# Kernel optimization log

Measured on AMD Instinct MI355X. Metric: run time of the kernel, lower is better.

## Reference

```python
import jax, jax.numpy as jnp
import numpy as np


def setup_inputs() -> dict:
    key = jax.random.key(0)
    kx, kw, kb = jax.random.split(key, 3)
    x = jax.random.normal(kx, (4, 2048, 4096), dtype=jnp.float32)
    weight = jax.random.normal(kw, (4096, 4096), dtype=jnp.float32) * 0.02
    bias = jax.random.normal(kb, (4096,), dtype=jnp.float32) * 0.02
    return {"x": x, "weight": weight, "bias": bias}


def _binarize_except_outliers(w):
    # Outlier mask from global weight stats (computed from w itself; in torch it
    # is cached after the first call but the values are identical every step).
    mean = jnp.mean(w)
    std = jnp.std(w, ddof=1)  # torch.std default is the unbiased estimator
    lower = mean - 1.96 * std
    upper = mean + 1.96 * std
    outliers = (w < lower) | (w > upper)
    keep = (~outliers).astype(w.dtype)
    # scaling_factor in the torch code: w[~outliers].abs().mean(-1) on the
    # flattened masked-select -> a single SCALAR, detached from the graph.
    scale = jax.lax.stop_gradient(jnp.sum(jnp.abs(w) * keep) / jnp.sum(keep))
    # NOTE: the torch code assigns STE-sign values and then immediately
    # overwrites them with w * scale, so the effective math is:
    w_bin = jnp.where(outliers, w, w * scale)
    return w_bin


def reference(x, weight, bias):
    w_bin = _binarize_except_outliers(weight)  # [out, in]
    # F.linear(x, w, b) = x @ w.T + b
    return jnp.einsum("bsi,oi->bso", x, w_bin) + bias
```

## Files before the change

kernel.cpp:

```cpp
#include <hip/hip_runtime.h>
#include <hip/hip_bf16.h>
#include <math.h>

#define MDIM 8192
#define NDIM 4096
#define KDIM 4096
#define WELEMS 16777216
#define XELEMS 33554432

typedef __attribute__((ext_vector_type(8))) short bf16x8;
typedef __attribute__((ext_vector_type(4))) float f32x4;

__device__ __forceinline__ unsigned short f2bf(float f) {
  unsigned int u = __float_as_uint(f);
  u += 0x7fffu + ((u >> 16) & 1u);
  return (unsigned short)(u >> 16);
}

__device__ __forceinline__ void gload16(const void* g, void* l) {
  __builtin_amdgcn_global_load_lds(
      (const __attribute__((address_space(1))) void*)g,
      (__attribute__((address_space(3))) void*)l, 16, 0, 0);
}


__device__ __forceinline__ float np_tree_reduce(const float* __restrict__ C, float* ls) {
  const int t = threadIdx.x;
  float v[16];
#pragma unroll
  for (int i = 0; i < 16; i++) v[i] = C[t * 16 + i];
#pragma unroll
  for (int n = 16; n > 1; n >>= 1)
    for (int i = 0; i < n / 2; i++) v[i] = v[2 * i] + v[2 * i + 1];
  __syncthreads();
  ls[t] = v[0];
  __syncthreads();
  for (int n = 256; n > 1; n >>= 1) {
    float s = 0.f;
    if (t < n / 2) s = ls[2 * t] + ls[2 * t + 1];
    __syncthreads();
    if (t < n / 2) ls[t] = s;
    __syncthreads();
  }
  float r = ls[0];
  __syncthreads();
  return r;
}

template <int MODE>
__global__ __launch_bounds__(256)
void np_stage1(const float* __restrict__ w, float* __restrict__ C,
               float* __restrict__ C2, const float* __restrict__ scal) {
  __shared__ float ls[32], ls2[32];
  const int t = threadIdx.x;
  const int leaf = t >> 3, j = t & 7;
  const size_t base = (size_t)blockIdx.x * 4096 + leaf * 128 + j;
  float mean = 0.f, lower = 0.f, upper = 0.f;
  if (MODE == 1) mean = scal[0];
  if (MODE == 2) { lower = scal[1]; upper = scal[2]; }
  float r = 0.f, r2 = 0.f;
#pragma unroll
  for (int s = 0; s < 16; s++) {
    float v = w[base + s * 8];
    float tv, tv2 = 0.f;
    if (MODE == 0) tv = v;
    else if (MODE == 1) { float x = v - mean; tv = __fmul_rn(x, x); }
    else {
      bool keep = !(v < lower || v > upper);
      tv = keep ? fabsf(v) : 0.f;
      tv2 = keep ? 1.f : 0.f;
    }
    if (s == 0) { r = tv; r2 = tv2; } else { r += tv; r2 += tv2; }
  }
  r += __shfl_xor(r, 1); r += __shfl_xor(r, 2); r += __shfl_xor(r, 4);
  if (MODE == 2) { r2 += __shfl_xor(r2, 1); r2 += __shfl_xor(r2, 2); r2 += __shfl_xor(r2, 4); }
  if (j == 0) { ls[leaf] = r; if (MODE == 2) ls2[leaf] = r2; }
  __syncthreads();
  if (t == 0) {
    float tmp[32];
    for (int i = 0; i < 32; i++) tmp[i] = ls[i];
    for (int n = 32; n > 1; n >>= 1)
      for (int i = 0; i < n / 2; i++) tmp[i] = tmp[2 * i] + tmp[2 * i + 1];
    C[blockIdx.x] = tmp[0];
    if (MODE == 2) {
      for (int i = 0; i < 32; i++) tmp[i] = ls2[i];
      for (int n = 32; n > 1; n >>= 1)
        for (int i = 0; i < n / 2; i++) tmp[i] = tmp[2 * i] + tmp[2 * i + 1];
      C2[blockIdx.x] = tmp[0];
    }
  }
}

template <int MODE>
__global__ __launch_bounds__(256)
void np_stage2(const float* __restrict__ C, const float* __restrict__ C2,
               float* __restrict__ scal) {
  __shared__ float ls[256], ls2[256];
  const int t = threadIdx.x;
  {
    float v[16];
    for (int i = 0; i < 16; i++) v[i] = C[t * 16 + i];
    for (int n = 16; n > 1; n >>= 1)
      for (int i = 0; i < n / 2; i++) v[i] = v[2 * i] + v[2 * i + 1];
    ls[t] = v[0];
    if (MODE == 2) {
      for (int i = 0; i < 16; i++) v[i] = C2[t * 16 + i];
      for (int n = 16; n > 1; n >>= 1)
        for (int i = 0; i < n / 2; i++) v[i] = v[2 * i] + v[2 * i + 1];
      ls2[t] = v[0];
    }
  }
  __syncthreads();
  if (t == 0) {
    float tmp[256];
    for (int i = 0; i < 256; i++) tmp[i] = ls[i];
    for (int n = 256; n > 1; n >>= 1)
      for (int i = 0; i < n / 2; i++) tmp[i] = tmp[2 * i] + tmp[2 * i + 1];
    float S = tmp[0];
    if (MODE == 0) {
      scal[0] = S / 16777216.0f;
    } else if (MODE == 1) {
      float var = S / 16777215.0f;
      float sd = sqrtf(var);
      float mean = scal[0];
      scal[1] = mean - __fmul_rn(1.96f, sd);
      scal[2] = mean + __fmul_rn(1.96f, sd);
    } else {
      for (int i = 0; i < 256; i++) tmp[i] = ls2[i];
      for (int n = 256; n > 1; n >>= 1)
        for (int i = 0; i < n / 2; i++) tmp[i] = tmp[2 * i] + tmp[2 * i + 1];
      scal[3] = S / tmp[0];
    }
  }
}

__device__ __forceinline__ void pack8(const float* __restrict__ p, unsigned short* dst,
                                      bool dobin, float lower, float upper, float scale) {
  float4 u = *(const float4*)p;
  float4 v = *(const float4*)(p + 4);
  float f[8] = {u.x, u.y, u.z, u.w, v.x, v.y, v.z, v.w};
  unsigned int r[4];
#pragma unroll
  for (int j = 0; j < 4; j++) {
    float a = f[2 * j], b = f[2 * j + 1];
    if (dobin) {
      bool oa = (a < lower) || (a > upper);
      bool ob = (b < lower) || (b > upper);
      a = oa ? a : __fmul_rn(a, scale);
      b = ob ? b : __fmul_rn(b, scale);
    }
    r[j] = (unsigned int)f2bf(a) | ((unsigned int)f2bf(b) << 16);
  }
  *(uint4*)dst = make_uint4(r[0], r[1], r[2], r[3]);
}

__global__ __launch_bounds__(256)
void convert_w(const float* __restrict__ w, unsigned short* __restrict__ wb,
               const float* __restrict__ scal) {
  float lower = scal[1], upper = scal[2], scale = scal[3];
  int tid = blockIdx.x * blockDim.x + threadIdx.x;
  int nth = gridDim.x * blockDim.x;
  int nc = WELEMS / 8;
  for (int i = tid; i < nc; i += nth)
    pack8(w + (size_t)i * 8, wb + (size_t)i * 8, true, lower, upper, scale);
}

__global__ __launch_bounds__(256)
void k2_var_convx(const float* __restrict__ w, const float* __restrict__ x,
                  const float* __restrict__ C1, float* __restrict__ C2,
                  unsigned short* __restrict__ xb) {
  if (blockIdx.x >= 4096) {
    int bid2 = blockIdx.x - 4096;
    for (int i = bid2 * 256 + threadIdx.x; i < XELEMS / 16; i += 2048 * 256)
      pack8(x + (size_t)i * 8, xb + (size_t)i * 8, false, 0.f, 0.f, 0.f);
    return;
  }
  __shared__ float red[256];
  __shared__ float ls[32];
  float mean = np_tree_reduce(C1, red) / 16777216.0f;
  const int t = threadIdx.x;
  const int leaf = t >> 3, j = t & 7;
  const size_t base = (size_t)blockIdx.x * 4096 + leaf * 128 + j;
  float r = 0.f;
#pragma unroll
  for (int s = 0; s < 16; s++) {
    float v = w[base + s * 8];
    float xv = v - mean;
    float tv = __fmul_rn(xv, xv);
    if (s == 0) r = tv; else r += tv;
  }
  r += __shfl_xor(r, 1); r += __shfl_xor(r, 2); r += __shfl_xor(r, 4);
  if (j == 0) ls[leaf] = r;
  __syncthreads();
  if (t == 0) {
    float tmp[32];
    for (int i = 0; i < 32; i++) tmp[i] = ls[i];
    for (int n = 32; n > 1; n >>= 1)
      for (int i = 0; i < n / 2; i++) tmp[i] = tmp[2 * i] + tmp[2 * i + 1];
    C2[blockIdx.x] = tmp[0];
  }
}

__global__ __launch_bounds__(256)
void k3_keep_convx(const float* __restrict__ w, const float* __restrict__ x,
                   const float* __restrict__ C1, const float* __restrict__ C2,
                   float* __restrict__ C3, float* __restrict__ C4,
                   unsigned short* __restrict__ xb) {
  if (blockIdx.x >= 4096) {
    int bid2 = blockIdx.x - 4096;
    for (int i = XELEMS / 16 + bid2 * 256 + threadIdx.x; i < XELEMS / 8; i += 2048 * 256)
      pack8(x + (size_t)i * 8, xb + (size_t)i * 8, false, 0.f, 0.f, 0.f);
    return;
  }
  __shared__ float red[256];
  __shared__ float ls[32], ls2[32];
  float S1 = np_tree_reduce(C1, red);
  float S2 = np_tree_reduce(C2, red);
  float mean = S1 / 16777216.0f;
  float sd = sqrtf(S2 / 16777215.0f);
  float lower = mean - __fmul_rn(1.96f, sd);
  float upper = mean + __fmul_rn(1.96f, sd);
  const int t = threadIdx.x;
  const int leaf = t >> 3, j = t & 7;
  const size_t base = (size_t)blockIdx.x * 4096 + leaf * 128 + j;
  float r = 0.f, r2 = 0.f;
#pragma unroll
  for (int s = 0; s < 16; s++) {
    float v = w[base + s * 8];
    bool keep = !(v < lower || v > upper);
    float tv = keep ? fabsf(v) : 0.f;
    float tv2 = keep ? 1.f : 0.f;
    if (s == 0) { r = tv; r2 = tv2; } else { r += tv; r2 += tv2; }
  }
  r += __shfl_xor(r, 1); r += __shfl_xor(r, 2); r += __shfl_xor(r, 4);
  r2 += __shfl_xor(r2, 1); r2 += __shfl_xor(r2, 2); r2 += __shfl_xor(r2, 4);
  if (j == 0) { ls[leaf] = r; ls2[leaf] = r2; }
  __syncthreads();
  if (t == 0) {
    float tmp[32];
    for (int i = 0; i < 32; i++) tmp[i] = ls[i];
    for (int n = 32; n > 1; n >>= 1)
      for (int i = 0; i < n / 2; i++) tmp[i] = tmp[2 * i] + tmp[2 * i + 1];
    C3[blockIdx.x] = tmp[0];
    for (int i = 0; i < 32; i++) tmp[i] = ls2[i];
    for (int n = 32; n > 1; n >>= 1)
      for (int i = 0; i < n / 2; i++) tmp[i] = tmp[2 * i] + tmp[2 * i + 1];
    C4[blockIdx.x] = tmp[0];
  }
}

__global__ __launch_bounds__(256)
void k4_convw(const float* __restrict__ w, const float* __restrict__ C1,
              const float* __restrict__ C2, const float* __restrict__ C3,
              const float* __restrict__ C4, unsigned short* __restrict__ wb) {
  __shared__ float red[256];
  float S1 = np_tree_reduce(C1, red);
  float S2 = np_tree_reduce(C2, red);
  float S3 = np_tree_reduce(C3, red);
  float S4 = np_tree_reduce(C4, red);
  float mean = S1 / 16777216.0f;
  float sd = sqrtf(S2 / 16777215.0f);
  float lower = mean - __fmul_rn(1.96f, sd);
  float upper = mean + __fmul_rn(1.96f, sd);
  float scale = S3 / S4;
  int tid = blockIdx.x * blockDim.x + threadIdx.x;
  int nth = gridDim.x * blockDim.x;
  int nc = WELEMS / 8;
  for (int i = tid; i < nc; i += nth)
    pack8(w + (size_t)i * 8, wb + (size_t)i * 8, true, lower, upper, scale);
}


#define VM(n) asm volatile("s_waitcnt vmcnt(" #n ")" ::: "memory")
#define PSYNC { asm volatile("" ::: "memory"); __builtin_amdgcn_s_barrier(); asm volatile("" ::: "memory"); }

#define RDA(slot, bufR, h) do { \
  slot[0][0] = *(const bf16x8*)&sA[bufR][wm][((2*(h)  )*16+fr)*64 + koo0]; \
  slot[0][1] = *(const bf16x8*)&sA[bufR][wm][((2*(h)  )*16+fr)*64 + koo1]; \
  slot[1][0] = *(const bf16x8*)&sA[bufR][wm][((2*(h)+1)*16+fr)*64 + koo0]; \
  slot[1][1] = *(const bf16x8*)&sA[bufR][wm][((2*(h)+1)*16+fr)*64 + koo1]; } while (0)

#define RDB2(slot, nf, bufR, bh) do { \
  slot[nf][0] = *(const bf16x8*)&sB[bufR][wnh][(wnq*64+(2*(bh)+(nf))*16+fr)*64 + koo0]; \
  slot[nf][1] = *(const bf16x8*)&sB[bufR][wnh][(wnq*64+(2*(bh)+(nf))*16+fr)*64 + koo1]; } while (0)

#define RDB4(slot, bufR, bh) do { RDB2(slot, 0, bufR, bh); RDB2(slot, 1, bufR, bh); } while (0)

#define MM8(AS, BSL, h, nh) do { \
  __builtin_amdgcn_s_setprio(1); \
  acc[2*(h)  ][2*(nh)  ] = __builtin_amdgcn_mfma_f32_16x16x32_bf16(AS[0][0], BSL[0][0], acc[2*(h)  ][2*(nh)  ], 0, 0, 0); \
  acc[2*(h)  ][2*(nh)+1] = __builtin_amdgcn_mfma_f32_16x16x32_bf16(AS[0][0], BSL[1][0], acc[2*(h)  ][2*(nh)+1], 0, 0, 0); \
  acc[2*(h)+1][2*(nh)  ] = __builtin_amdgcn_mfma_f32_16x16x32_bf16(AS[1][0], BSL[0][0], acc[2*(h)+1][2*(nh)  ], 0, 0, 0); \
  acc[2*(h)+1][2*(nh)+1] = __builtin_amdgcn_mfma_f32_16x16x32_bf16(AS[1][0], BSL[1][0], acc[2*(h)+1][2*(nh)+1], 0, 0, 0); \
  acc[2*(h)  ][2*(nh)  ] = __builtin_amdgcn_mfma_f32_16x16x32_bf16(AS[0][1], BSL[0][1], acc[2*(h)  ][2*(nh)  ], 0, 0, 0); \
  acc[2*(h)  ][2*(nh)+1] = __builtin_amdgcn_mfma_f32_16x16x32_bf16(AS[0][1], BSL[1][1], acc[2*(h)  ][2*(nh)+1], 0, 0, 0); \
  acc[2*(h)+1][2*(nh)  ] = __builtin_amdgcn_mfma_f32_16x16x32_bf16(AS[1][1], BSL[0][1], acc[2*(h)+1][2*(nh)  ], 0, 0, 0); \
  acc[2*(h)+1][2*(nh)+1] = __builtin_amdgcn_mfma_f32_16x16x32_bf16(AS[1][1], BSL[1][1], acc[2*(h)+1][2*(nh)+1], 0, 0, 0); \
  __builtin_amdgcn_s_setprio(0); } while (0)

#define STGA(buf, q, kadd) do { \
  gload16(xbp + aofA[0][q] + (kadd), &sA[buf][0][(q)*4096 + t8]); \
  gload16(xbp + aofA[1][q] + (kadd), &sA[buf][1][(q)*4096 + t8]); } while (0)
#define STGB(buf, h, kadd) do { \
  gload16(wbp + bofB[h][0] + (kadd), &sB[buf][h][t8]); \
  gload16(wbp + bofB[h][1] + (kadd), &sB[buf][h][4096 + t8]); } while (0)

#define TILE(BR, BW, BF, BS_, KADD) do { \
   PSYNC; RDB2(BS_, 0, BR, 1); STGA(BW, 0, KADD); MM8(aA, BF, 0, 0); \
   PSYNC; RDB2(BS_, 1, BR, 1); STGB(BW, 0, KADD); MM8(aB, BF, 1, 0); VM(4); \
   PSYNC; RDA(aC, BR, 2); STGB(BW, 1, KADD); MM8(aB, BS_, 1, 1); \
   PSYNC; RDA(aB, BR, 3); STGA(BW, 1, KADD); MM8(aA, BS_, 0, 1); \
   PSYNC; MM8(aC, BS_, 2, 1); VM(6); \
   PSYNC; RDA(aA, BW, 0); MM8(aB, BS_, 3, 1); VM(2); \
   PSYNC; MM8(aB, BF, 3, 0); RDB4(BS_, BW, 0); \
   PSYNC; MM8(aC, BF, 2, 0); RDA(aB, BW, 1); } while (0)

__global__ __launch_bounds__(512, 2)
void gemm256(const unsigned short* __restrict__ xbp, const unsigned short* __restrict__ wbp,
             const float* __restrict__ bias, float* __restrict__ out) {
  __shared__ unsigned short sA[2][2][8192];
  __shared__ unsigned short sB[2][2][8192];

  const int bid = blockIdx.x;
  const int swz = (bid & 7) * 64 + (bid >> 3);
  const int bm = swz >> 4, bn = swz & 15;

  const int t = threadIdx.x;
  const int lane = t & 63;
  const int wid = t >> 6;
  const int wm = wid >> 2, wn = wid & 3;
  const int wnh = wn >> 1, wnq = wn & 1;
  const int fr = lane & 15;
  const int ko = (lane >> 4) * 8;
  const int xr = (fr & 7) << 3;
  const int koo0 = ko ^ xr;
  const int koo1 = (32 + ko) ^ xr;

  const int t8 = t * 8;
  const int rl = t >> 3;
  const int cs = ((t & 7) * 8) ^ ((rl & 7) << 3);
  unsigned int aofA[2][2], bofB[2][2];
#pragma unroll
  for (int h = 0; h < 2; h++)
#pragma unroll
    for (int q = 0; q < 2; q++) {
      aofA[h][q] = (unsigned int)((bm * 256 + h * 128 + q * 64 + rl) * KDIM + cs);
      bofB[h][q] = (unsigned int)((bn * 256 + h * 128 + q * 64 + rl) * KDIM + cs);
    }

  f32x4 acc[8][4];
#pragma unroll
  for (int i = 0; i < 8; i++)
#pragma unroll
    for (int j = 0; j < 4; j++) acc[i][j] = {0.f, 0.f, 0.f, 0.f};

  bf16x8 aA[2][2], aB[2][2], aC[2][2], bs0[2][2], bs1[2][2];

  STGA(0, 0, 0); STGB(0, 0, 0); STGB(0, 1, 0); STGA(0, 1, 0);
  VM(2); PSYNC;
  RDA(aA, 0, 0); RDA(aB, 0, 1); RDB4(bs0, 0, 0);

  for (int it = 0; it < 31; ++it) {
    TILE(0, 1, bs0, bs1, 64);
    TILE(1, 0, bs1, bs0, 128);
#pragma unroll
    for (int h = 0; h < 2; h++)
#pragma unroll
      for (int q = 0; q < 2; q++) { aofA[h][q] += 128; bofB[h][q] += 128; }
  }
  TILE(0, 1, bs0, bs1, 64);
   PSYNC; RDB2(bs0, 0, 1, 1); MM8(aA, bs1, 0, 0);
   PSYNC; RDB2(bs0, 1, 1, 1); MM8(aB, bs1, 1, 0); VM(0);
   PSYNC; RDA(aC, 1, 2); MM8(aB, bs0, 1, 1);
   PSYNC; RDA(aB, 1, 3); MM8(aA, bs0, 0, 1);
   PSYNC; MM8(aC, bs0, 2, 1);
   PSYNC; MM8(aB, bs0, 3, 1);
   PSYNC; MM8(aB, bs1, 3, 0);
   PSYNC; MM8(aC, bs1, 2, 0);

#pragma unroll
  for (int nn = 0; nn < 4; ++nn) {
    const int col = bn * 256 + wn * 64 + nn * 16 + (lane & 15);
    const float bv = bias[col];
#pragma unroll
    for (int m = 0; m < 8; ++m) {
      const int row0 = bm * 256 + wm * 128 + m * 16 + (lane >> 4) * 4;
#pragma unroll
      for (int q = 0; q < 4; ++q)
        out[(size_t)(row0 + q) * NDIM + col] = acc[m][nn][q] + bv;
    }
  }
}

template <bool A_BF16, bool B_BF16>
__global__ __launch_bounds__(256)
void gemm_bt(const void* __restrict__ Av, const void* __restrict__ Bv,
             const float* __restrict__ bias, float* __restrict__ out,
             const float* __restrict__ scal) {
  __shared__ unsigned short sAt[2][128 * 32];
  __shared__ unsigned short sBt[2][128 * 32];
  float lower = 0.f, upper = 0.f, scale = 0.f;
  if constexpr (!B_BF16) { lower = scal[1]; upper = scal[2]; scale = scal[3]; }
  const unsigned short* Ab = (const unsigned short*)Av;
  const float* Af = (const float*)Av;
  const unsigned short* Bb = (const unsigned short*)Bv;
  const float* Bf = (const float*)Bv;
  int bid = blockIdx.x;
  int swz = (bid & 7) * 256 + (bid >> 3);
  int bm = swz >> 5, bn = swz & 31;
  const int t = threadIdx.x, lane = t & 63, wid = t >> 6;
  const int wm = wid >> 1, wn = wid & 1;
  const int e0 = t * 8, e1 = e0 + 2048;
  const size_t aOff0 = (size_t)(bm * 128 + (e0 >> 5)) * KDIM + (e0 & 31);
  const size_t aOff1 = (size_t)(bm * 128 + (e1 >> 5)) * KDIM + (e1 & 31);
  const size_t bOff0 = (size_t)(bn * 128 + (e0 >> 5)) * KDIM + (e0 & 31);
  const size_t bOff1 = (size_t)(bn * 128 + (e1 >> 5)) * KDIM + (e1 & 31);
  f32x4 acc[4][4];
#pragma unroll
  for (int i = 0; i < 4; i++)
#pragma unroll
    for (int j = 0; j < 4; j++) acc[i][j] = {0.f, 0.f, 0.f, 0.f};
  auto stage = [&](int buf, int k0) {
    if constexpr (A_BF16) {
      gload16(Ab + aOff0 + k0, &sAt[buf][e0]);
      gload16(Ab + aOff1 + k0, &sAt[buf][e1]);
    } else {
      pack8(Af + aOff0 + k0, &sAt[buf][e0], false, 0.f, 0.f, 0.f);
      pack8(Af + aOff1 + k0, &sAt[buf][e1], false, 0.f, 0.f, 0.f);
    }
    if constexpr (B_BF16) {
      gload16(Bb + bOff0 + k0, &sBt[buf][e0]);
      gload16(Bb + bOff1 + k0, &sBt[buf][e1]);
    } else {
      pack8(Bf + bOff0 + k0, &sBt[buf][e0], true, lower, upper, scale);
      pack8(Bf + bOff1 + k0, &sBt[buf][e1], true, lower, upper, scale);
    }
  };
  stage(0, 0);
  const int NT = KDIM / 32;
  const int ko = (lane >> 4) * 8, fr = lane & 15;
  for (int tt = 0; tt < NT; ++tt) {
    int cur = tt & 1;
    __syncthreads();
    if (tt + 1 < NT) stage(cur ^ 1, (tt + 1) * 32);
    bf16x8 a[4], b[4];
#pragma unroll
    for (int i = 0; i < 4; i++) {
      a[i] = *(const bf16x8*)&sAt[cur][(wm * 64 + i * 16 + fr) * 32 + ko];
      b[i] = *(const bf16x8*)&sBt[cur][(wn * 64 + i * 16 + fr) * 32 + ko];
    }
#pragma unroll
    for (int i = 0; i < 4; i++)
#pragma unroll
      for (int j = 0; j < 4; j++)
        acc[i][j] = __builtin_amdgcn_mfma_f32_16x16x32_bf16(a[i], b[j], acc[i][j], 0, 0, 0);
  }
  const int colbase = bn * 128 + wn * 64 + (lane & 15);
  const int rowbase = bm * 128 + wm * 64 + (lane >> 4) * 4;
#pragma unroll
  for (int j = 0; j < 4; j++) {
    int col = colbase + j * 16;
    float bv = bias[col];
#pragma unroll
    for (int i = 0; i < 4; i++) {
      int row0 = rowbase + i * 16;
#pragma unroll
      for (int q = 0; q < 4; q++)
        out[(size_t)(row0 + q) * NDIM + col] = acc[i][j][q] + bv;
    }
  }
}

extern "C" void kernel_launch(void* const* d_in, const int* in_sizes, int n_in,
                              void* d_out, int out_size, void* d_ws, size_t ws_size,
                              hipStream_t stream) {
  const float* x = (const float*)d_in[0];
  const float* w = (const float*)d_in[1];
  const float* bias = (const float*)d_in[2];
  float* out = (float*)d_out;
  char* ws = (char*)d_ws;

  const size_t xb_b = (size_t)XELEMS * 2;
  const size_t wb_b = (size_t)WELEMS * 2;
  const size_t c_b = 4 * 4096 * sizeof(float);
  const bool full = ws_size >= xb_b + wb_b + c_b + 64;
  const bool wonly = !full && ws_size >= wb_b + c_b + 64;

  unsigned short *xb = nullptr, *wb = nullptr;
  float *C1, *scal;
  if (full) {
    xb = (unsigned short*)ws;
    wb = (unsigned short*)(ws + xb_b);
    C1 = (float*)(ws + xb_b + wb_b);
  } else if (wonly) {
    wb = (unsigned short*)ws;
    C1 = (float*)(ws + wb_b);
  } else {
    C1 = (float*)ws;
  }
  float* C2 = C1 + 4096;
  float* C3 = C2 + 4096;
  float* C4 = C3 + 4096;
  scal = C4 + 4096;

  if (full) {
    np_stage1<0><<<dim3(4096), dim3(256), 0, stream>>>(w, C1, nullptr, scal);
    k2_var_convx<<<dim3(6144), dim3(256), 0, stream>>>(w, x, C1, C2, xb);
    k3_keep_convx<<<dim3(6144), dim3(256), 0, stream>>>(w, x, C1, C2, C3, C4, xb);
    k4_convw<<<dim3(2048), dim3(256), 0, stream>>>(w, C1, C2, C3, C4, wb);
    gemm256<<<dim3(512), dim3(512), 0, stream>>>(xb, wb, bias, out);
  } else {
    np_stage1<0><<<dim3(4096), dim3(256), 0, stream>>>(w, C1, nullptr, scal);
    np_stage2<0><<<dim3(1), dim3(256), 0, stream>>>(C1, nullptr, scal);
    np_stage1<1><<<dim3(4096), dim3(256), 0, stream>>>(w, C2, nullptr, scal);
    np_stage2<1><<<dim3(1), dim3(256), 0, stream>>>(C2, nullptr, scal);
    np_stage1<2><<<dim3(4096), dim3(256), 0, stream>>>(w, C3, C4, scal);
    np_stage2<2><<<dim3(1), dim3(256), 0, stream>>>(C3, C4, scal);
    if (wonly) {
      convert_w<<<dim3(2048), dim3(256), 0, stream>>>(w, wb, scal);
      gemm_bt<false, true><<<dim3(2048), dim3(256), 0, stream>>>(x, wb, bias, out, scal);
    } else {
      gemm_bt<false, false><<<dim3(2048), dim3(256), 0, stream>>>(x, w, bias, out, scal);
    }
  }
}
```

Before: 382.7 us.

## Switch GEMM main loop to four-stage K=32 LDS pipeline

Replaces the double-buffered K=64 LDS tiles with a four-buffer ring of K=32 tiles, prefetching three stages ahead with direct global-to-LDS loads. It also changes the LDS swizzle for 32-wide rows and regroups the MFMA schedule into four phases per tile. The aim is to hide global memory latency with deeper prefetch while keeping total LDS size the same. The cost is twice as many barriers per unit of K and a more intricate waitcnt schedule.

```diff
diff --git a/kernel.cpp b/kernel.cpp
--- a/kernel.cpp
+++ b/kernel.cpp
@@ -22,7 +22,6 @@
       (const __attribute__((address_space(1))) void*)g,
       (__attribute__((address_space(3))) void*)l, 16, 0, 0);
 }
-
 
 __device__ __forceinline__ float np_tree_reduce(const float* __restrict__ C, float* ls) {
   const int t = threadIdx.x;
@@ -274,52 +273,46 @@
 #define VM(n) asm volatile("s_waitcnt vmcnt(" #n ")" ::: "memory")
 #define PSYNC { asm volatile("" ::: "memory"); __builtin_amdgcn_s_barrier(); asm volatile("" ::: "memory"); }
 
-#define RDA(slot, bufR, h) do { \
-  slot[0][0] = *(const bf16x8*)&sA[bufR][wm][((2*(h)  )*16+fr)*64 + koo0]; \
-  slot[0][1] = *(const bf16x8*)&sA[bufR][wm][((2*(h)  )*16+fr)*64 + koo1]; \
-  slot[1][0] = *(const bf16x8*)&sA[bufR][wm][((2*(h)+1)*16+fr)*64 + koo0]; \
-  slot[1][1] = *(const bf16x8*)&sA[bufR][wm][((2*(h)+1)*16+fr)*64 + koo1]; } while (0)
-
-#define RDB2(slot, nf, bufR, bh) do { \
-  slot[nf][0] = *(const bf16x8*)&sB[bufR][wnh][(wnq*64+(2*(bh)+(nf))*16+fr)*64 + koo0]; \
-  slot[nf][1] = *(const bf16x8*)&sB[bufR][wnh][(wnq*64+(2*(bh)+(nf))*16+fr)*64 + koo1]; } while (0)
-
-#define RDB4(slot, bufR, bh) do { RDB2(slot, 0, bufR, bh); RDB2(slot, 1, bufR, bh); } while (0)
-
-#define MM8(AS, BSL, h, nh) do { \
+#define RDA4(slot, buf, h) do { \
+  slot[0] = *(const bf16x8*)&sA[buf][wm][((h)*64 +  0 + fr)*32 + koo]; \
+  slot[1] = *(const bf16x8*)&sA[buf][wm][((h)*64 + 16 + fr)*32 + koo]; \
+  slot[2] = *(const bf16x8*)&sA[buf][wm][((h)*64 + 32 + fr)*32 + koo]; \
+  slot[3] = *(const bf16x8*)&sA[buf][wm][((h)*64 + 48 + fr)*32 + koo]; } while (0)
+
+#define RDB2(slot, buf, bh) do { \
+  slot[0] = *(const bf16x8*)&sB[buf][wnh][(wnq*64 + ((bh)*2+0)*16 + fr)*32 + koo]; \
+  slot[1] = *(const bf16x8*)&sB[buf][wnh][(wnq*64 + ((bh)*2+1)*16 + fr)*32 + koo]; } while (0)
+
+#define MMH(AS, BS, mh, n2) do { \
   __builtin_amdgcn_s_setprio(1); \
-  acc[2*(h)  ][2*(nh)  ] = __builtin_amdgcn_mfma_f32_16x16x32_bf16(AS[0][0], BSL[0][0], acc[2*(h)  ][2*(nh)  ], 0, 0, 0); \
-  acc[2*(h)  ][2*(nh)+1] = __builtin_amdgcn_mfma_f32_16x16x32_bf16(AS[0][0], BSL[1][0], acc[2*(h)  ][2*(nh)+1], 0, 0, 0); \
-  acc[2*(h)+1][2*(nh)  ] = __builtin_amdgcn_mfma_f32_16x16x32_bf16(AS[1][0], BSL[0][0], acc[2*(h)+1][2*(nh)  ], 0, 0, 0); \
-  acc[2*(h)+1][2*(nh)+1] = __builtin_amdgcn_mfma_f32_16x16x32_bf16(AS[1][0], BSL[1][0], acc[2*(h)+1][2*(nh)+1], 0, 0, 0); \
-  acc[2*(h)  ][2*(nh)  ] = __builtin_amdgcn_mfma_f32_16x16x32_bf16(AS[0][1], BSL[0][1], acc[2*(h)  ][2*(nh)  ], 0, 0, 0); \
-  acc[2*(h)  ][2*(nh)+1] = __builtin_amdgcn_mfma_f32_16x16x32_bf16(AS[0][1], BSL[1][1], acc[2*(h)  ][2*(nh)+1], 0, 0, 0); \
-  acc[2*(h)+1][2*(nh)  ] = __builtin_amdgcn_mfma_f32_16x16x32_bf16(AS[1][1], BSL[0][1], acc[2*(h)+1][2*(nh)  ], 0, 0, 0); \
-  acc[2*(h)+1][2*(nh)+1] = __builtin_amdgcn_mfma_f32_16x16x32_bf16(AS[1][1], BSL[1][1], acc[2*(h)+1][2*(nh)+1], 0, 0, 0); \
+  acc[(mh)*4+0][(n2)*2+0] = __builtin_amdgcn_mfma_f32_16x16x32_bf16(AS[0], BS[0], acc[(mh)*4+0][(n2)*2+0], 0, 0, 0); \
+  acc[(mh)*4+0][(n2)*2+1] = __builtin_amdgcn_mfma_f32_16x16x32_bf16(AS[0], BS[1], acc[(mh)*4+0][(n2)*2+1], 0, 0, 0); \
+  acc[(mh)*4+1][(n2)*2+0] = __builtin_amdgcn_mfma_f32_16x16x32_bf16(AS[1], BS[0], acc[(mh)*4+1][(n2)*2+0], 0, 0, 0); \
+  acc[(mh)*4+1][(n2)*2+1] = __builtin_amdgcn_mfma_f32_16x16x32_bf16(AS[1], BS[1], acc[(mh)*4+1][(n2)*2+1], 0, 0, 0); \
+  acc[(mh)*4+2][(n2)*2+0] = __builtin_amdgcn_mfma_f32_16x16x32_bf16(AS[2], BS[0], acc[(mh)*4+2][(n2)*2+0], 0, 0, 0); \
+  acc[(mh)*4+2][(n2)*2+1] = __builtin_amdgcn_mfma_f32_16x16x32_bf16(AS[2], BS[1], acc[(mh)*4+2][(n2)*2+1], 0, 0, 0); \
+  acc[(mh)*4+3][(n2)*2+0] = __builtin_amdgcn_mfma_f32_16x16x32_bf16(AS[3], BS[0], acc[(mh)*4+3][(n2)*2+0], 0, 0, 0); \
+  acc[(mh)*4+3][(n2)*2+1] = __builtin_amdgcn_mfma_f32_16x16x32_bf16(AS[3], BS[1], acc[(mh)*4+3][(n2)*2+1], 0, 0, 0); \
   __builtin_amdgcn_s_setprio(0); } while (0)
 
-#define STGA(buf, q, kadd) do { \
-  gload16(xbp + aofA[0][q] + (kadd), &sA[buf][0][(q)*4096 + t8]); \
-  gload16(xbp + aofA[1][q] + (kadd), &sA[buf][1][(q)*4096 + t8]); } while (0)
-#define STGB(buf, h, kadd) do { \
-  gload16(wbp + bofB[h][0] + (kadd), &sB[buf][h][t8]); \
-  gload16(wbp + bofB[h][1] + (kadd), &sB[buf][h][4096 + t8]); } while (0)
-
-#define TILE(BR, BW, BF, BS_, KADD) do { \
-   PSYNC; RDB2(BS_, 0, BR, 1); STGA(BW, 0, KADD); MM8(aA, BF, 0, 0); \
-   PSYNC; RDB2(BS_, 1, BR, 1); STGB(BW, 0, KADD); MM8(aB, BF, 1, 0); VM(4); \
-   PSYNC; RDA(aC, BR, 2); STGB(BW, 1, KADD); MM8(aB, BS_, 1, 1); \
-   PSYNC; RDA(aB, BR, 3); STGA(BW, 1, KADD); MM8(aA, BS_, 0, 1); \
-   PSYNC; MM8(aC, BS_, 2, 1); VM(6); \
-   PSYNC; RDA(aA, BW, 0); MM8(aB, BS_, 3, 1); VM(2); \
-   PSYNC; MM8(aB, BF, 3, 0); RDB4(BS_, BW, 0); \
-   PSYNC; MM8(aC, BF, 2, 0); RDA(aB, BW, 1); } while (0)
+#define STGA32(buf, kadd) do { \
+  gload16(xbp + aof0 + (kadd), &sA[buf][0][t8]); \
+  gload16(xbp + aof1 + (kadd), &sA[buf][1][t8]); } while (0)
+#define STGB32(buf, kadd) do { \
+  gload16(wbp + bof0 + (kadd), &sB[buf][0][t8]); \
+  gload16(wbp + bof1 + (kadd), &sB[buf][1][t8]); } while (0)
+
+#define TILE32(CUR, NXT, STGBUF, BC, BO, DOSTG, KS, DOVM, VMN, DONEXT) do { \
+   PSYNC; RDB2(BO, CUR, 1); if (DOSTG) STGA32(STGBUF, KS); MMH(aX, BC, 0, 0); \
+   PSYNC; RDA4(aY, CUR, 1); MMH(aX, BO, 0, 1); if (DOVM) VM(VMN); \
+   PSYNC; if (DONEXT) RDA4(aX, NXT, 0); if (DOSTG) STGB32(STGBUF, KS); MMH(aY, BO, 1, 1); \
+   PSYNC; if (DONEXT) RDB2(BO, NXT, 0); MMH(aY, BC, 1, 0); } while (0)
 
 __global__ __launch_bounds__(512, 2)
 void gemm256(const unsigned short* __restrict__ xbp, const unsigned short* __restrict__ wbp,
              const float* __restrict__ bias, float* __restrict__ out) {
-  __shared__ unsigned short sA[2][2][8192];
-  __shared__ unsigned short sB[2][2][8192];
+  __shared__ unsigned short sA[4][2][4096];
+  __shared__ unsigned short sB[4][2][4096];
 
   const int bid = blockIdx.x;
   const int swz = (bid & 7) * 64 + (bid >> 3);
@@ -331,22 +324,16 @@
   const int wm = wid >> 2, wn = wid & 3;
   const int wnh = wn >> 1, wnq = wn & 1;
   const int fr = lane & 15;
-  const int ko = (lane >> 4) * 8;
-  const int xr = (fr & 7) << 3;
-  const int koo0 = ko ^ xr;
-  const int koo1 = (32 + ko) ^ xr;
+  const int kh = lane >> 4;
+  const int koo = 8 * (kh ^ ((fr >> 1) & 3));
 
   const int t8 = t * 8;
-  const int rl = t >> 3;
-  const int cs = ((t & 7) * 8) ^ ((rl & 7) << 3);
-  unsigned int aofA[2][2], bofB[2][2];
-#pragma unroll
-  for (int h = 0; h < 2; h++)
-#pragma unroll
-    for (int q = 0; q < 2; q++) {
-      aofA[h][q] = (unsigned int)((bm * 256 + h * 128 + q * 64 + rl) * KDIM + cs);
-      bofB[h][q] = (unsigned int)((bn * 256 + h * 128 + q * 64 + rl) * KDIM + cs);
-    }
+  const int rl = t >> 2;
+  const int cs = 8 * ((t & 3) ^ ((rl >> 1) & 3));
+  unsigned int aof0 = (unsigned int)((bm * 256 + 0 * 128 + rl) * KDIM + cs);
+  unsigned int aof1 = (unsigned int)((bm * 256 + 1 * 128 + rl) * KDIM + cs);
+  unsigned int bof0 = (unsigned int)((bn * 256 + 0 * 128 + rl) * KDIM + cs);
+  unsigned int bof1 = (unsigned int)((bn * 256 + 1 * 128 + rl) * KDIM + cs);
 
   f32x4 acc[8][4];
 #pragma unroll
@@ -354,29 +341,25 @@
 #pragma unroll
     for (int j = 0; j < 4; j++) acc[i][j] = {0.f, 0.f, 0.f, 0.f};
 
-  bf16x8 aA[2][2], aB[2][2], aC[2][2], bs0[2][2], bs1[2][2];
-
-  STGA(0, 0, 0); STGB(0, 0, 0); STGB(0, 1, 0); STGA(0, 1, 0);
-  VM(2); PSYNC;
-  RDA(aA, 0, 0); RDA(aB, 0, 1); RDB4(bs0, 0, 0);
-
-  for (int it = 0; it < 31; ++it) {
-    TILE(0, 1, bs0, bs1, 64);
-    TILE(1, 0, bs1, bs0, 128);
-#pragma unroll
-    for (int h = 0; h < 2; h++)
-#pragma unroll
-      for (int q = 0; q < 2; q++) { aofA[h][q] += 128; bofB[h][q] += 128; }
-  }
-  TILE(0, 1, bs0, bs1, 64);
-   PSYNC; RDB2(bs0, 0, 1, 1); MM8(aA, bs1, 0, 0);
-   PSYNC; RDB2(bs0, 1, 1, 1); MM8(aB, bs1, 1, 0); VM(0);
-   PSYNC; RDA(aC, 1, 2); MM8(aB, bs0, 1, 1);
-   PSYNC; RDA(aB, 1, 3); MM8(aA, bs0, 0, 1);
-   PSYNC; MM8(aC, bs0, 2, 1);
-   PSYNC; MM8(aB, bs0, 3, 1);
-   PSYNC; MM8(aB, bs1, 3, 0);
-   PSYNC; MM8(aC, bs1, 2, 0);
+  bf16x8 aX[4], aY[4], b0[2], b1[2];
+
+  STGA32(0, 0);  STGB32(0, 0);
+  STGA32(1, 32); STGB32(1, 32);
+  STGA32(2, 64); STGB32(2, 64);
+  VM(8); PSYNC;
+  RDA4(aX, 0, 0); RDB2(b0, 0, 0);
+
+  for (int g = 0; g < 31; ++g) {
+    TILE32(0, 1, 3, b0, b1, true, 96,  true, 6, true);
+    TILE32(1, 2, 0, b1, b0, true, 128, true, 6, true);
+    TILE32(2, 3, 1, b0, b1, true, 160, true, 6, true);
+    TILE32(3, 0, 2, b1, b0, true, 192, true, 6, true);
+    aof0 += 128; aof1 += 128; bof0 += 128; bof1 += 128;
+  }
+  TILE32(0, 1, 3, b0, b1, true, 96, true, 6, true);
+  TILE32(1, 2, 0, b1, b0, false, 0, true, 4, true);
+  TILE32(2, 3, 0, b0, b1, false, 0, true, 0, true);
+  TILE32(3, 0, 0, b1, b0, false, 0, false, 0, false);
 
 #pragma unroll
   for (int nn = 0; nn < 4; ++nn) {
```

New measurement: 376.4 us (median of 2 runs). About the same (-1.6%).

## Switch main GEMM to 32x32x16 MFMA with restructured LDS pipeline

Applied to the files above, without the earlier changes.

Replaces the 16x16x32 bf16 MFMA tiling in the 256x256 GEMM with 32x32x16 MFMAs. Each wave now holds a 4x2 grid of 32x32 accumulators, and the LDS fragment reads and swizzle offsets are rewritten to match. The K-loop is rebuilt as a simpler per-128-K iteration with explicit prefetch staging, lgkmcnt waits and more barriers. The larger MFMA shape needs fewer LDS reads per flop, at the cost of a different schedule with more barriers that may overlap memory and compute less well.

```diff
diff --git a/kernel.cpp b/kernel.cpp
--- a/kernel.cpp
+++ b/kernel.cpp
@@ -10,6 +10,7 @@
 
 typedef __attribute__((ext_vector_type(8))) short bf16x8;
 typedef __attribute__((ext_vector_type(4))) float f32x4;
+typedef __attribute__((ext_vector_type(16))) float f32x16;
 
 __device__ __forceinline__ unsigned short f2bf(float f) {
   unsigned int u = __float_as_uint(f);
@@ -22,7 +23,6 @@
       (const __attribute__((address_space(1))) void*)g,
       (__attribute__((address_space(3))) void*)l, 16, 0, 0);
 }
-
 
 __device__ __forceinline__ float np_tree_reduce(const float* __restrict__ C, float* ls) {
   const int t = threadIdx.x;
@@ -272,30 +272,35 @@
 
 
 #define VM(n) asm volatile("s_waitcnt vmcnt(" #n ")" ::: "memory")
+#define LGK8 asm volatile("s_waitcnt lgkmcnt(8)" ::: "memory")
 #define PSYNC { asm volatile("" ::: "memory"); __builtin_amdgcn_s_barrier(); asm volatile("" ::: "memory"); }
 
-#define RDA(slot, bufR, h) do { \
-  slot[0][0] = *(const bf16x8*)&sA[bufR][wm][((2*(h)  )*16+fr)*64 + koo0]; \
-  slot[0][1] = *(const bf16x8*)&sA[bufR][wm][((2*(h)  )*16+fr)*64 + koo1]; \
-  slot[1][0] = *(const bf16x8*)&sA[bufR][wm][((2*(h)+1)*16+fr)*64 + koo0]; \
-  slot[1][1] = *(const bf16x8*)&sA[bufR][wm][((2*(h)+1)*16+fr)*64 + koo1]; } while (0)
-
-#define RDB2(slot, nf, bufR, bh) do { \
-  slot[nf][0] = *(const bf16x8*)&sB[bufR][wnh][(wnq*64+(2*(bh)+(nf))*16+fr)*64 + koo0]; \
-  slot[nf][1] = *(const bf16x8*)&sB[bufR][wnh][(wnq*64+(2*(bh)+(nf))*16+fr)*64 + koo1]; } while (0)
-
-#define RDB4(slot, bufR, bh) do { RDB2(slot, 0, bufR, bh); RDB2(slot, 1, bufR, bh); } while (0)
-
-#define MM8(AS, BSL, h, nh) do { \
+#define RDA(buf, mh) do { \
+  a[0][0] = *(const bf16x8*)&sA[buf][wm][((mh)*64 +  0 + l31)*64 + koo0]; \
+  a[0][1] = *(const bf16x8*)&sA[buf][wm][((mh)*64 +  0 + l31)*64 + koo1]; \
+  a[0][2] = *(const bf16x8*)&sA[buf][wm][((mh)*64 +  0 + l31)*64 + koo2]; \
+  a[0][3] = *(const bf16x8*)&sA[buf][wm][((mh)*64 +  0 + l31)*64 + koo3]; \
+  a[1][0] = *(const bf16x8*)&sA[buf][wm][((mh)*64 + 32 + l31)*64 + koo0]; \
+  a[1][1] = *(const bf16x8*)&sA[buf][wm][((mh)*64 + 32 + l31)*64 + koo1]; \
+  a[1][2] = *(const bf16x8*)&sA[buf][wm][((mh)*64 + 32 + l31)*64 + koo2]; \
+  a[1][3] = *(const bf16x8*)&sA[buf][wm][((mh)*64 + 32 + l31)*64 + koo3]; } while (0)
+
+#define RDB(slot, buf, nh) do { \
+  slot[0] = *(const bf16x8*)&sB[buf][wnh][(wnq*64 + (nh)*32 + l31)*64 + koo0]; \
+  slot[1] = *(const bf16x8*)&sB[buf][wnh][(wnq*64 + (nh)*32 + l31)*64 + koo1]; \
+  slot[2] = *(const bf16x8*)&sB[buf][wnh][(wnq*64 + (nh)*32 + l31)*64 + koo2]; \
+  slot[3] = *(const bf16x8*)&sB[buf][wnh][(wnq*64 + (nh)*32 + l31)*64 + koo3]; } while (0)
+
+#define MM(mh, nh, BS) do { \
   __builtin_amdgcn_s_setprio(1); \
-  acc[2*(h)  ][2*(nh)  ] = __builtin_amdgcn_mfma_f32_16x16x32_bf16(AS[0][0], BSL[0][0], acc[2*(h)  ][2*(nh)  ], 0, 0, 0); \
-  acc[2*(h)  ][2*(nh)+1] = __builtin_amdgcn_mfma_f32_16x16x32_bf16(AS[0][0], BSL[1][0], acc[2*(h)  ][2*(nh)+1], 0, 0, 0); \
-  acc[2*(h)+1][2*(nh)  ] = __builtin_amdgcn_mfma_f32_16x16x32_bf16(AS[1][0], BSL[0][0], acc[2*(h)+1][2*(nh)  ], 0, 0, 0); \
-  acc[2*(h)+1][2*(nh)+1] = __builtin_amdgcn_mfma_f32_16x16x32_bf16(AS[1][0], BSL[1][0], acc[2*(h)+1][2*(nh)+1], 0, 0, 0); \
-  acc[2*(h)  ][2*(nh)  ] = __builtin_amdgcn_mfma_f32_16x16x32_bf16(AS[0][1], BSL[0][1], acc[2*(h)  ][2*(nh)  ], 0, 0, 0); \
-  acc[2*(h)  ][2*(nh)+1] = __builtin_amdgcn_mfma_f32_16x16x32_bf16(AS[0][1], BSL[1][1], acc[2*(h)  ][2*(nh)+1], 0, 0, 0); \
-  acc[2*(h)+1][2*(nh)  ] = __builtin_amdgcn_mfma_f32_16x16x32_bf16(AS[1][1], BSL[0][1], acc[2*(h)+1][2*(nh)  ], 0, 0, 0); \
-  acc[2*(h)+1][2*(nh)+1] = __builtin_amdgcn_mfma_f32_16x16x32_bf16(AS[1][1], BSL[1][1], acc[2*(h)+1][2*(nh)+1], 0, 0, 0); \
+  acc[(mh)*2+0][nh] = __builtin_amdgcn_mfma_f32_32x32x16_bf16(a[0][0], BS[0], acc[(mh)*2+0][nh], 0, 0, 0); \
+  acc[(mh)*2+1][nh] = __builtin_amdgcn_mfma_f32_32x32x16_bf16(a[1][0], BS[0], acc[(mh)*2+1][nh], 0, 0, 0); \
+  acc[(mh)*2+0][nh] = __builtin_amdgcn_mfma_f32_32x32x16_bf16(a[0][1], BS[1], acc[(mh)*2+0][nh], 0, 0, 0); \
+  acc[(mh)*2+1][nh] = __builtin_amdgcn_mfma_f32_32x32x16_bf16(a[1][1], BS[1], acc[(mh)*2+1][nh], 0, 0, 0); \
+  acc[(mh)*2+0][nh] = __builtin_amdgcn_mfma_f32_32x32x16_bf16(a[0][2], BS[2], acc[(mh)*2+0][nh], 0, 0, 0); \
+  acc[(mh)*2+1][nh] = __builtin_amdgcn_mfma_f32_32x32x16_bf16(a[1][2], BS[2], acc[(mh)*2+1][nh], 0, 0, 0); \
+  acc[(mh)*2+0][nh] = __builtin_amdgcn_mfma_f32_32x32x16_bf16(a[0][3], BS[3], acc[(mh)*2+0][nh], 0, 0, 0); \
+  acc[(mh)*2+1][nh] = __builtin_amdgcn_mfma_f32_32x32x16_bf16(a[1][3], BS[3], acc[(mh)*2+1][nh], 0, 0, 0); \
   __builtin_amdgcn_s_setprio(0); } while (0)
 
 #define STGA(buf, q, kadd) do { \
@@ -305,16 +310,6 @@
   gload16(wbp + bofB[h][0] + (kadd), &sB[buf][h][t8]); \
   gload16(wbp + bofB[h][1] + (kadd), &sB[buf][h][4096 + t8]); } while (0)
 
-#define TILE(BR, BW, BF, BS_, KADD) do { \
-   PSYNC; RDB2(BS_, 0, BR, 1); STGA(BW, 0, KADD); MM8(aA, BF, 0, 0); \
-   PSYNC; RDB2(BS_, 1, BR, 1); STGB(BW, 0, KADD); MM8(aB, BF, 1, 0); VM(4); \
-   PSYNC; RDA(aC, BR, 2); STGB(BW, 1, KADD); MM8(aB, BS_, 1, 1); \
-   PSYNC; RDA(aB, BR, 3); STGA(BW, 1, KADD); MM8(aA, BS_, 0, 1); \
-   PSYNC; MM8(aC, BS_, 2, 1); VM(6); \
-   PSYNC; RDA(aA, BW, 0); MM8(aB, BS_, 3, 1); VM(2); \
-   PSYNC; MM8(aB, BF, 3, 0); RDB4(BS_, BW, 0); \
-   PSYNC; MM8(aC, BF, 2, 0); RDA(aB, BW, 1); } while (0)
-
 __global__ __launch_bounds__(512, 2)
 void gemm256(const unsigned short* __restrict__ xbp, const unsigned short* __restrict__ wbp,
              const float* __restrict__ bias, float* __restrict__ out) {
@@ -330,11 +325,13 @@
   const int wid = t >> 6;
   const int wm = wid >> 2, wn = wid & 3;
   const int wnh = wn >> 1, wnq = wn & 1;
-  const int fr = lane & 15;
-  const int ko = (lane >> 4) * 8;
-  const int xr = (fr & 7) << 3;
-  const int koo0 = ko ^ xr;
-  const int koo1 = (32 + ko) ^ xr;
+  const int l31 = lane & 31;
+  const int l7 = lane & 7;
+  const int kh2 = lane >> 5;
+  const int koo0 = 8 * ((0 + kh2) ^ l7);
+  const int koo1 = 8 * ((2 + kh2) ^ l7);
+  const int koo2 = 8 * ((4 + kh2) ^ l7);
+  const int koo3 = 8 * ((6 + kh2) ^ l7);
 
   const int t8 = t * 8;
   const int rl = t >> 3;
@@ -348,46 +345,78 @@
       bofB[h][q] = (unsigned int)((bn * 256 + h * 128 + q * 64 + rl) * KDIM + cs);
     }
 
-  f32x4 acc[8][4];
-#pragma unroll
-  for (int i = 0; i < 8; i++)
-#pragma unroll
-    for (int j = 0; j < 4; j++) acc[i][j] = {0.f, 0.f, 0.f, 0.f};
-
-  bf16x8 aA[2][2], aB[2][2], aC[2][2], bs0[2][2], bs1[2][2];
+  f32x16 acc[4][2];
+#pragma unroll
+  for (int i = 0; i < 4; i++)
+#pragma unroll
+    for (int j = 0; j < 2; j++)
+#pragma unroll
+      for (int q = 0; q < 16; q++) acc[i][j][q] = 0.f;
+
+  bf16x8 a[2][4], b0[4], b1[4];
 
   STGA(0, 0, 0); STGB(0, 0, 0); STGB(0, 1, 0); STGA(0, 1, 0);
-  VM(2); PSYNC;
-  RDA(aA, 0, 0); RDA(aB, 0, 1); RDB4(bs0, 0, 0);
-
-  for (int it = 0; it < 31; ++it) {
-    TILE(0, 1, bs0, bs1, 64);
-    TILE(1, 0, bs1, bs0, 128);
-#pragma unroll
-    for (int h = 0; h < 2; h++)
-#pragma unroll
-      for (int q = 0; q < 2; q++) { aofA[h][q] += 128; bofB[h][q] += 128; }
-  }
-  TILE(0, 1, bs0, bs1, 64);
-   PSYNC; RDB2(bs0, 0, 1, 1); MM8(aA, bs1, 0, 0);
-   PSYNC; RDB2(bs0, 1, 1, 1); MM8(aB, bs1, 1, 0); VM(0);
-   PSYNC; RDA(aC, 1, 2); MM8(aB, bs0, 1, 1);
-   PSYNC; RDA(aB, 1, 3); MM8(aA, bs0, 0, 1);
-   PSYNC; MM8(aC, bs0, 2, 1);
-   PSYNC; MM8(aB, bs0, 3, 1);
-   PSYNC; MM8(aB, bs1, 3, 0);
-   PSYNC; MM8(aC, bs1, 2, 0);
-
-#pragma unroll
-  for (int nn = 0; nn < 4; ++nn) {
-    const int col = bn * 256 + wn * 64 + nn * 16 + (lane & 15);
+  STGB(1, 0, 64); STGB(1, 1, 64); STGA(1, 0, 64);
+  VM(6); PSYNC;
+
+  const int NIT = KDIM / 128;
+  for (int it = 0; it < NIT; ++it) {
+    const bool last = (it == NIT - 1);
+    const int kuB = it * 128 + 64;
+    const int kuN = kuB + 64;
+    const int kuL = kuB + 128;
+
+    RDA(0, 0); RDB(b0, 0, 0);
+    STGA(1, 1, kuB);
+    LGK8; PSYNC;
+    MM(0, 0, b0); PSYNC;
+
+    RDB(b1, 0, 1);
+    PSYNC;
+    MM(0, 1, b1); PSYNC;
+
+    RDA(0, 1);
+    if (!last) { STGB(0, 0, kuN); STGB(0, 1, kuN); }
+    PSYNC;
+    MM(1, 1, b1); PSYNC;
+
+    if (!last) STGA(0, 0, kuN);
+    if (last) { VM(0); } else { VM(6); }
+    PSYNC;
+    MM(1, 0, b0); PSYNC;
+
+    RDA(1, 0); RDB(b0, 1, 0);
+    if (!last) STGA(0, 1, kuN);
+    LGK8; PSYNC;
+    MM(0, 0, b0); PSYNC;
+
+    RDB(b1, 1, 1);
+    PSYNC;
+    MM(0, 1, b1); PSYNC;
+
+    RDA(1, 1);
+    if (!last) { STGB(1, 0, kuL); STGB(1, 1, kuL); }
+    PSYNC;
+    MM(1, 1, b1); PSYNC;
+
+    if (!last) { STGA(1, 0, kuL); VM(6); }
+    PSYNC;
+    MM(1, 0, b0); PSYNC;
+  }
+
+  const int rquad = kh2 * 4;
+#pragma unroll
+  for (int nh = 0; nh < 2; ++nh) {
+    const int col = bn * 256 + wn * 64 + nh * 32 + l31;
     const float bv = bias[col];
 #pragma unroll
-    for (int m = 0; m < 8; ++m) {
-      const int row0 = bm * 256 + wm * 128 + m * 16 + (lane >> 4) * 4;
-#pragma unroll
-      for (int q = 0; q < 4; ++q)
-        out[(size_t)(row0 + q) * NDIM + col] = acc[m][nn][q] + bv;
+    for (int mi = 0; mi < 4; ++mi) {
+      const int row0 = bm * 256 + wm * 128 + mi * 32 + rquad;
+#pragma unroll
+      for (int q = 0; q < 16; ++q) {
+        const int row = row0 + (q & 3) + 8 * (q >> 2);
+        out[(size_t)row * NDIM + col] = acc[mi][nh][q] + bv;
+      }
     }
   }
 }
```

Result: slower. 394.1 us (+3.0%).
